# Kernel tuning notes

Hardware: AMD Instinct MI355X
Metric: run time of the kernel (lower is better)

The kernel has to match this reference:

```python
import jax, jax.numpy as jnp
import numpy as np

B, S, DM, H = 4, 4096, 1024, 16
HD = DM // H

def setup_inputs() -> dict:
    key = jax.random.key(0)
    ks = jax.random.split(key, 9)
    sc = 1.0 / np.sqrt(DM)
    return {
        "x": jax.random.normal(ks[0], (B, S, DM), dtype=jnp.float32),
        "Wq": jax.random.normal(ks[1], (DM, DM), dtype=jnp.float32) * sc,
        "bq": jnp.zeros((DM,), dtype=jnp.float32),
        "Wk": jax.random.normal(ks[2], (DM, DM), dtype=jnp.float32) * sc,
        "bk": jnp.zeros((DM,), dtype=jnp.float32),
        "Wv": jax.random.normal(ks[3], (DM, DM), dtype=jnp.float32) * sc,
        "bv": jnp.zeros((DM,), dtype=jnp.float32),
        "Wo": jax.random.normal(ks[4], (DM, DM), dtype=jnp.float32) * sc,
        "bo": jnp.zeros((DM,), dtype=jnp.float32),
    }

def _heads(t):
    # [B,S,DM] -> [B,H,S,HD]
    return t.reshape(B, S, H, HD).transpose(0, 2, 1, 3)

def reference(x, Wq, bq, Wk, bk, Wv, bv, Wo, bo):
    q = _heads(x @ Wq.T + bq)
    k = _heads(x @ Wk.T + bk)
    v = _heads(x @ Wv.T + bv)
    q = jax.nn.elu(q) + 1.0  # positive feature map
    k = jax.nn.elu(k) + 1.0
    # kv aggregation: [B,H,HD,HD]
    kv = jnp.einsum('bhsd,bhse->bhde', k, v)
    qkv = jnp.einsum('bhsd,bhde->bhse', q, kv)  # [B,H,S,HD]
    k_sum = k.sum(axis=2)  # [B,H,HD]
    normalizer = jnp.einsum('bhsd,bhd->bhs', q, k_sum) + 1e-6
    out = qkv / normalizer[..., None]
    out = out.transpose(0, 2, 1, 3).reshape(B, S, DM)
    return out @ Wo.T + bo  # dropout is identity in eval
```

## Files before the change

kernel.cpp:

```cpp
#include <hip/hip_runtime.h>
#include <math.h>

#define NROWS  16384
#define DMODEL 1024
#define NHEAD  16
#define HDIM   64
#define SEQ    4096
#define NBATCH 4
#define NBH    64
#define SCHUNK 16
#define M1     1048576u

typedef __attribute__((ext_vector_type(8))) short bf16x8;
typedef __attribute__((ext_vector_type(4))) float f32x4;

__device__ __forceinline__ unsigned short f2bf(float f) {
    unsigned u = __float_as_uint(f);
    u += 0x7FFFu + ((u >> 16) & 1u);
    return (unsigned short)(u >> 16);
}
__device__ __forceinline__ float bf2f(unsigned short h) {
    return __uint_as_float((unsigned)h << 16);
}

__device__ __forceinline__ void gload16(const void* g, void* l) {
    __builtin_amdgcn_global_load_lds(
        (const __attribute__((address_space(1))) unsigned int*)g,
        (__attribute__((address_space(3))) unsigned int*)l, 16, 0, 0);
}

__global__ __launch_bounds__(256)
void split_pair(const float* __restrict__ a, unsigned short* __restrict__ hi,
                unsigned short* __restrict__ lo, int n4)
{
    int i = blockIdx.x * 256 + threadIdx.x;
    const int stride = gridDim.x * 256;
    for (; i < n4; i += stride) {
        const float4 v = ((const float4*)a)[i];
        ushort4 H, L;
        H.x = f2bf(v.x); L.x = f2bf(v.x - bf2f(H.x));
        H.y = f2bf(v.y); L.y = f2bf(v.y - bf2f(H.y));
        H.z = f2bf(v.z); L.z = f2bf(v.z - bf2f(H.z));
        H.w = f2bf(v.w); L.w = f2bf(v.w - bf2f(H.w));
        ((ushort4*)hi)[i] = H;
        ((ushort4*)lo)[i] = L;
    }
}

__global__ __launch_bounds__(256)
void split_w4(const float* __restrict__ a0, const float* __restrict__ a1,
              const float* __restrict__ a2, const float* __restrict__ a3,
              unsigned short* __restrict__ dst)
{
    const int y = blockIdx.y;
    const float* src = (y == 0) ? a0 : (y == 1) ? a1 : (y == 2) ? a2 : a3;
    unsigned short* hi = dst + (size_t)y * 2u * M1;
    unsigned short* lo = hi + M1;
    const int i = blockIdx.x * 256 + threadIdx.x;
    const float4 v = ((const float4*)src)[i];
    ushort4 H, L;
    H.x = f2bf(v.x); L.x = f2bf(v.x - bf2f(H.x));
    H.y = f2bf(v.y); L.y = f2bf(v.y - bf2f(H.y));
    H.z = f2bf(v.z); L.z = f2bf(v.z - bf2f(H.z));
    H.w = f2bf(v.w); L.w = f2bf(v.w - bf2f(H.w));
    ((ushort4*)hi)[i] = H;
    ((ushort4*)lo)[i] = L;
}

template<int ELU>
__global__ __launch_bounds__(512)
void gemm_split8(const unsigned short* __restrict__ Ah, const unsigned short* __restrict__ Al,
                 const unsigned short* __restrict__ Wh, const unsigned short* __restrict__ Wl,
                 const float* __restrict__ bias, float* __restrict__ C)
{
    __shared__ unsigned short lds[2 * 32768];
    const int t    = threadIdx.x;
    const int lane = t & 63;
    const int wv   = t >> 6;
    const int wr   = wv >> 2;
    const int wcn  = wv & 3;

    const int bid  = blockIdx.x;
    const int swz  = ((bid & 7) << 5) | (bid >> 3);
    const int am0  = (swz >> 2) * 256;
    const int bn0  = (swz & 3) * 256;

    const int fr   = lane & 15;
    const int j0   = lane >> 4;
    const unsigned fro = (unsigned)((j0 * 16 + fr) * 8);
    const int srcr = lane & 15;
    const int srcc = (lane >> 4) * 8;

    f32x4 acc[8][4];
#pragma unroll
    for (int i = 0; i < 8; ++i)
#pragma unroll
        for (int j = 0; j < 4; ++j)
#pragma unroll
            for (int e = 0; e < 4; ++e) acc[i][j][e] = 0.f;

    auto stage = [&](int ph, int k0, unsigned wb) {
        const unsigned short* gs = (ph == 0) ? Ah : (ph == 1) ? Al : (ph == 2) ? Wh : Wl;
        const int rbase = (ph < 2) ? am0 : bn0;
#pragma unroll
        for (int c = 0; c < 2; ++c) {
            const int grow = rbase + c * 128 + wv * 16 + srcr;
            gload16(gs + (size_t)grow * DMODEL + k0 + srcc,
                    (unsigned short*)&lds[wb + (unsigned)ph * 8192u + (unsigned)(c * 8 + wv) * 512u]);
        }
    };

#pragma unroll
    for (int ph = 0; ph < 4; ++ph) stage(ph, 0, 0u);
    __syncthreads();

    for (int ks = 0; ks < 32; ++ks) {
        const unsigned rb = (ks & 1) ? 32768u : 0u;
        const unsigned wb = rb ^ 32768u;
        const int k0n = (ks + 1) * 32;
        const bool pf = (ks < 31);

        bf16x8 bh[4], bl[4];
#pragma unroll
        for (int ph = 0; ph < 4; ++ph) {
            if (ph == 0) {
#pragma unroll
                for (int j = 0; j < 4; ++j) {
                    const unsigned ch = (unsigned)(wcn * 4 + j) * 512u;
                    bh[j] = *(const bf16x8*)&lds[rb + 16384u + ch + fro];
                    bl[j] = *(const bf16x8*)&lds[rb + 24576u + ch + fro];
                }
            }
            bf16x8 a_h[2], a_l[2];
#pragma unroll
            for (int i2 = 0; i2 < 2; ++i2) {
                const unsigned ch = (unsigned)(wr * 8 + ph * 2 + i2) * 512u;
                a_h[i2] = *(const bf16x8*)&lds[rb + ch + fro];
                a_l[i2] = *(const bf16x8*)&lds[rb + 8192u + ch + fro];
            }
            if (pf) stage(ph, k0n, wb);
            __builtin_amdgcn_s_barrier();
            __builtin_amdgcn_s_setprio(1);
#pragma unroll
            for (int i2 = 0; i2 < 2; ++i2)
#pragma unroll
                for (int j = 0; j < 4; ++j) {
                    acc[ph * 2 + i2][j] = __builtin_amdgcn_mfma_f32_16x16x32_bf16(a_h[i2], bh[j], acc[ph * 2 + i2][j], 0, 0, 0);
                    acc[ph * 2 + i2][j] = __builtin_amdgcn_mfma_f32_16x16x32_bf16(a_h[i2], bl[j], acc[ph * 2 + i2][j], 0, 0, 0);
                    acc[ph * 2 + i2][j] = __builtin_amdgcn_mfma_f32_16x16x32_bf16(a_l[i2], bh[j], acc[ph * 2 + i2][j], 0, 0, 0);
                }
            __builtin_amdgcn_s_setprio(0);
            if (ph < 3) __builtin_amdgcn_s_barrier();
        }
        __syncthreads();
    }

    const int crow0 = am0 + wr * 128 + (lane >> 4) * 4;
    const int ccol0 = bn0 + wcn * 64 + fr;
#pragma unroll
    for (int j = 0; j < 4; ++j) {
        const int col = ccol0 + j * 16;
        const float bv = bias[col];
#pragma unroll
        for (int i = 0; i < 8; ++i) {
            const int row = crow0 + i * 16;
#pragma unroll
            for (int r = 0; r < 4; ++r) {
                float v = acc[i][j][r] + bv;
                if (ELU) v = (v > 0.f) ? (v + 1.f) : __expf(v);
                C[(size_t)(row + r) * DMODEL + col] = v;
            }
        }
    }
}

__global__ __launch_bounds__(512)
void kv_partial(const float* __restrict__ k, const float* __restrict__ v,
                float* __restrict__ kvp, float* __restrict__ ksp)
{
    __shared__ float Ks[32][64];
    __shared__ float Vs[32][64];
    const int t  = threadIdx.x;
    const int bh = blockIdx.x;
    const int b  = bh >> 4;
    const int h  = bh & 15;
    const int sc = blockIdx.y;
    const int d  = t & 63;
    const int e0 = (t >> 6) * 8;

    float acc[8];
#pragma unroll
    for (int j = 0; j < 8; ++j) acc[j] = 0.f;
    float ks = 0.f;

    const size_t rowbase = (size_t)b * SEQ;
    const int sbeg = sc * (SEQ / SCHUNK);
    const int send = sbeg + (SEQ / SCHUNK);
    const int lrow = t >> 4;
    const int lc4  = (t & 15) * 4;

    for (int s0 = sbeg; s0 < send; s0 += 32) {
        const size_t g = (rowbase + s0 + lrow) * DMODEL + h * HDIM + lc4;
        *(float4*)&Ks[lrow][lc4] = *(const float4*)&k[g];
        *(float4*)&Vs[lrow][lc4] = *(const float4*)&v[g];
        __syncthreads();
#pragma unroll 8
        for (int sp = 0; sp < 32; ++sp) {
            const float kd = Ks[sp][d];
            if (t < 64) ks += Ks[sp][t];
            const float4 v0 = *(const float4*)&Vs[sp][e0 + 0];
            const float4 v1 = *(const float4*)&Vs[sp][e0 + 4];
            acc[0] = fmaf(kd, v0.x, acc[0]);  acc[1] = fmaf(kd, v0.y, acc[1]);
            acc[2] = fmaf(kd, v0.z, acc[2]);  acc[3] = fmaf(kd, v0.w, acc[3]);
            acc[4] = fmaf(kd, v1.x, acc[4]);  acc[5] = fmaf(kd, v1.y, acc[5]);
            acc[6] = fmaf(kd, v1.z, acc[6]);  acc[7] = fmaf(kd, v1.w, acc[7]);
        }
        __syncthreads();
    }

    const size_t base = ((size_t)sc * NBH + bh) * HDIM;
    float4 o0; o0.x = acc[0]; o0.y = acc[1]; o0.z = acc[2]; o0.w = acc[3];
    float4 o1; o1.x = acc[4]; o1.y = acc[5]; o1.z = acc[6]; o1.w = acc[7];
    *(float4*)&kvp[(base + d) * HDIM + e0 + 0] = o0;
    *(float4*)&kvp[(base + d) * HDIM + e0 + 4] = o1;
    if (t < 64) ksp[base + t] = ks;
}

__global__ __launch_bounds__(256)
void kv_reduce(const float* __restrict__ kvp, const float* __restrict__ ksp,
               float* __restrict__ kv, float* __restrict__ ksum)
{
    const int i = blockIdx.x * 256 + threadIdx.x;
    const int NKV = NBH * HDIM * HDIM;
    if (i < NKV) {
        float s = 0.f;
#pragma unroll
        for (int c = 0; c < SCHUNK; ++c) s += kvp[(size_t)c * NKV + i];
        kv[i] = s;
    }
    if (i < NBH * HDIM) {
        float s = 0.f;
#pragma unroll
        for (int c = 0; c < SCHUNK; ++c) s += ksp[(size_t)c * NBH * HDIM + i];
        ksum[i] = s;
    }
}

__global__ __launch_bounds__(256)
void qkv_norm(const float* __restrict__ q, const float* __restrict__ kv,
              const float* __restrict__ ksum,
              unsigned short* __restrict__ ah, unsigned short* __restrict__ al)
{
    __shared__ float Qs[64][68];
    __shared__ float KVs[64][64];
    __shared__ float kss[64];
    const int t  = threadIdx.x;
    const int s0 = blockIdx.x * 64;
    const int b  = blockIdx.y;
    const int h  = blockIdx.z;
    const int bh = b * NHEAD + h;

#pragma unroll
    for (int i = 0; i < 4; ++i) {
        const int idx = i * 256 + t;
        const int row = idx >> 4;
        const int c4  = (idx & 15) * 4;
        const float4 vq = *(const float4*)&q[((size_t)b * SEQ + s0 + row) * DMODEL + h * HDIM + c4];
        *(float4*)&Qs[row][c4] = vq;
        *(float4*)&((float*)KVs)[idx * 4] = *(const float4*)&kv[(size_t)bh * HDIM * HDIM + idx * 4];
    }
    if (t < 64) kss[t] = ksum[(size_t)bh * HDIM + t];
    __syncthreads();

    const int r  = t >> 2;
    const int e0 = (t & 3) * 16;
    float out[16];
#pragma unroll
    for (int j = 0; j < 16; ++j) out[j] = 0.f;
    float nrm = 0.f;

#pragma unroll 8
    for (int d = 0; d < 64; ++d) {
        const float qd = Qs[r][d];
        nrm = fmaf(qd, kss[d], nrm);
        const float4 k0 = *(const float4*)&KVs[d][e0 + 0];
        const float4 k1 = *(const float4*)&KVs[d][e0 + 4];
        const float4 k2 = *(const float4*)&KVs[d][e0 + 8];
        const float4 k3 = *(const float4*)&KVs[d][e0 + 12];
        out[0]  = fmaf(qd, k0.x, out[0]);  out[1]  = fmaf(qd, k0.y, out[1]);
        out[2]  = fmaf(qd, k0.z, out[2]);  out[3]  = fmaf(qd, k0.w, out[3]);
        out[4]  = fmaf(qd, k1.x, out[4]);  out[5]  = fmaf(qd, k1.y, out[5]);
        out[6]  = fmaf(qd, k1.z, out[6]);  out[7]  = fmaf(qd, k1.w, out[7]);
        out[8]  = fmaf(qd, k2.x, out[8]);  out[9]  = fmaf(qd, k2.y, out[9]);
        out[10] = fmaf(qd, k2.z, out[10]); out[11] = fmaf(qd, k2.w, out[11]);
        out[12] = fmaf(qd, k3.x, out[12]); out[13] = fmaf(qd, k3.y, out[13]);
        out[14] = fmaf(qd, k3.z, out[14]); out[15] = fmaf(qd, k3.w, out[15]);
    }

    const float inv = 1.f / (nrm + 1e-6f);
    const size_t gbase = ((size_t)b * SEQ + s0 + r) * DMODEL + h * HDIM + e0;
#pragma unroll
    for (int g4 = 0; g4 < 4; ++g4) {
        ushort4 H, L;
        const float v0 = out[g4*4+0] * inv;
        const float v1 = out[g4*4+1] * inv;
        const float v2 = out[g4*4+2] * inv;
        const float v3 = out[g4*4+3] * inv;
        H.x = f2bf(v0); L.x = f2bf(v0 - bf2f(H.x));
        H.y = f2bf(v1); L.y = f2bf(v1 - bf2f(H.y));
        H.z = f2bf(v2); L.z = f2bf(v2 - bf2f(H.z));
        H.w = f2bf(v3); L.w = f2bf(v3 - bf2f(H.w));
        *(ushort4*)&ah[gbase + g4 * 4] = H;
        *(ushort4*)&al[gbase + g4 * 4] = L;
    }
}

extern "C" void kernel_launch(void* const* d_in, const int* in_sizes, int n_in,
                              void* d_out, int out_size, void* d_ws, size_t ws_size,
                              hipStream_t stream)
{
    const float* x  = (const float*)d_in[0];
    const float* Wq = (const float*)d_in[1];
    const float* bq = (const float*)d_in[2];
    const float* Wk = (const float*)d_in[3];
    const float* bk = (const float*)d_in[4];
    const float* Wv = (const float*)d_in[5];
    const float* bv = (const float*)d_in[6];
    const float* Wo = (const float*)d_in[7];
    const float* bo = (const float*)d_in[8];

    unsigned short* xh = (unsigned short*)d_ws;
    unsigned short* xl = xh + (size_t)NROWS * DMODEL;
    unsigned short* wsp = xl + (size_t)NROWS * DMODEL;
    float* buf0 = (float*)(wsp + 8u * M1);
    float* kv   = buf0 + (size_t)NROWS * DMODEL;
    float* ksum = kv + NBH * HDIM * HDIM;
    float* kvp  = ksum + NBH * HDIM;
    float* ksp  = kvp + (size_t)SCHUNK * NBH * HDIM * HDIM;
    float* vbuf = (float*)d_out;

    const dim3 gg(256);
    const int n4x = NROWS * DMODEL / 4;

    split_w4<<<dim3(1024, 4), 256, 0, stream>>>(Wq, Wk, Wv, Wo, wsp);
    split_pair<<<4096, 256, 0, stream>>>(x, xh, xl, n4x);
    gemm_split8<1><<<gg, 512, 0, stream>>>(xh, xl, wsp + 2u * M1, wsp + 3u * M1, bk, buf0);
    gemm_split8<0><<<gg, 512, 0, stream>>>(xh, xl, wsp + 4u * M1, wsp + 5u * M1, bv, vbuf);
    kv_partial<<<dim3(NBH, SCHUNK), 512, 0, stream>>>(buf0, vbuf, kvp, ksp);
    kv_reduce<<<1024, 256, 0, stream>>>(kvp, ksp, kv, ksum);
    gemm_split8<1><<<gg, 512, 0, stream>>>(xh, xl, wsp, wsp + M1, bq, buf0);
    qkv_norm<<<dim3(SEQ / 64, NBATCH, NHEAD), 256, 0, stream>>>(buf0, kv, ksum, xh, xl);
    gemm_split8<0><<<gg, 512, 0, stream>>>(xh, xl, wsp + 6u * M1, wsp + 7u * M1, bo, (float*)d_out);
}
```

Before: 488.2 us.

## Rewrite split-bf16 GEMM with triple-buffered LDS, smaller tiles, fused K/V launch

The GEMM moves to 256x128 tiles and a three-stage LDS ring. Loads are issued two k-steps ahead and gated by explicit vmcnt waits, replacing the per-phase barriers of the old double-buffered loop. Weights are packed into contiguous hi and lo arrays, so the K and V projections run as one launch over a concatenated 2048-column weight, with ELU and the output destination chosen per column block. Smaller tiles give twice as many blocks for better occupancy and load balance, at the cost of more operand re-reads and a larger LDS footprint per block.

```diff
diff --git a/kernel.cpp b/kernel.cpp
--- a/kernel.cpp
+++ b/kernel.cpp
@@ -13,6 +13,10 @@
 
 typedef __attribute__((ext_vector_type(8))) short bf16x8;
 typedef __attribute__((ext_vector_type(4))) float f32x4;
+
+#define VMCNT(N) asm volatile("s_waitcnt vmcnt(" #N ")" ::: "memory")
+#define BAR() do { asm volatile("" ::: "memory"); __builtin_amdgcn_s_barrier(); \
+                   asm volatile("" ::: "memory"); } while (0)
 
 __device__ __forceinline__ unsigned short f2bf(float f) {
     unsigned u = __float_as_uint(f);
@@ -50,12 +54,10 @@
 __global__ __launch_bounds__(256)
 void split_w4(const float* __restrict__ a0, const float* __restrict__ a1,
               const float* __restrict__ a2, const float* __restrict__ a3,
-              unsigned short* __restrict__ dst)
+              unsigned short* __restrict__ hib, unsigned short* __restrict__ lob)
 {
     const int y = blockIdx.y;
     const float* src = (y == 0) ? a0 : (y == 1) ? a1 : (y == 2) ? a2 : a3;
-    unsigned short* hi = dst + (size_t)y * 2u * M1;
-    unsigned short* lo = hi + M1;
     const int i = blockIdx.x * 256 + threadIdx.x;
     const float4 v = ((const float4*)src)[i];
     ushort4 H, L;
@@ -63,27 +65,32 @@
     H.y = f2bf(v.y); L.y = f2bf(v.y - bf2f(H.y));
     H.z = f2bf(v.z); L.z = f2bf(v.z - bf2f(H.z));
     H.w = f2bf(v.w); L.w = f2bf(v.w - bf2f(H.w));
-    ((ushort4*)hi)[i] = H;
-    ((ushort4*)lo)[i] = L;
-}
-
-template<int ELU>
+    const size_t o = (size_t)y * M1 + (size_t)i * 4;
+    *(ushort4*)&hib[o] = H;
+    *(ushort4*)&lob[o] = L;
+}
+
+template<int MODE>
 __global__ __launch_bounds__(512)
-void gemm_split8(const unsigned short* __restrict__ Ah, const unsigned short* __restrict__ Al,
-                 const unsigned short* __restrict__ Wh, const unsigned short* __restrict__ Wl,
-                 const float* __restrict__ bias, float* __restrict__ C)
-{
-    __shared__ unsigned short lds[2 * 32768];
+void gemm_t3(const unsigned short* __restrict__ Ah, const unsigned short* __restrict__ Al,
+             const unsigned short* __restrict__ WhB, const unsigned short* __restrict__ WlB,
+             const float* __restrict__ bias0, const float* __restrict__ bias1,
+             float* __restrict__ C0, float* __restrict__ C1, int nbs, int wrow0)
+{
+    __shared__ unsigned short lds[73728];
     const int t    = threadIdx.x;
     const int lane = t & 63;
     const int wv   = t >> 6;
-    const int wr   = wv >> 2;
-    const int wcn  = wv & 3;
+    const int wr   = wv >> 1;
+    const int wcn  = wv & 1;
 
     const int bid  = blockIdx.x;
-    const int swz  = ((bid & 7) << 5) | (bid >> 3);
-    const int am0  = (swz >> 2) * 256;
-    const int bn0  = (swz & 3) * 256;
+    const int swz  = (bid & 7) * ((int)gridDim.x >> 3) + (bid >> 3);
+    const int NBm  = (1 << nbs) - 1;
+    const int mb   = swz >> nbs;
+    const int nb   = swz & NBm;
+    const int am0  = mb * 256;
+    const int bn0g = wrow0 + nb * 128;
 
     const int fr   = lane & 15;
     const int j0   = lane >> 4;
@@ -91,84 +98,93 @@
     const int srcr = lane & 15;
     const int srcc = (lane >> 4) * 8;
 
-    f32x4 acc[8][4];
-#pragma unroll
-    for (int i = 0; i < 8; ++i)
+    f32x4 acc[4][4];
+#pragma unroll
+    for (int i = 0; i < 4; ++i)
 #pragma unroll
         for (int j = 0; j < 4; ++j)
 #pragma unroll
             for (int e = 0; e < 4; ++e) acc[i][j][e] = 0.f;
 
-    auto stage = [&](int ph, int k0, unsigned wb) {
-        const unsigned short* gs = (ph == 0) ? Ah : (ph == 1) ? Al : (ph == 2) ? Wh : Wl;
-        const int rbase = (ph < 2) ? am0 : bn0;
+    auto stage_full = [&](int kt, unsigned wb) {
 #pragma unroll
         for (int c = 0; c < 2; ++c) {
-            const int grow = rbase + c * 128 + wv * 16 + srcr;
-            gload16(gs + (size_t)grow * DMODEL + k0 + srcc,
-                    (unsigned short*)&lds[wb + (unsigned)ph * 8192u + (unsigned)(c * 8 + wv) * 512u]);
-        }
+            const int ch = wv * 2 + c;
+            const size_t ga = (size_t)(am0 + ch * 16 + srcr) * DMODEL + kt * 32 + srcc;
+            gload16(Ah + ga, (unsigned short*)&lds[wb + (unsigned)ch * 512u]);
+            gload16(Al + ga, (unsigned short*)&lds[wb + 8192u + (unsigned)ch * 512u]);
+        }
+        const size_t gb = (size_t)(bn0g + wv * 16 + srcr) * DMODEL + kt * 32 + srcc;
+        gload16(WhB + gb, (unsigned short*)&lds[wb + 16384u + (unsigned)wv * 512u]);
+        gload16(WlB + gb, (unsigned short*)&lds[wb + 20480u + (unsigned)wv * 512u]);
     };
 
-#pragma unroll
-    for (int ph = 0; ph < 4; ++ph) stage(ph, 0, 0u);
-    __syncthreads();
-
-    for (int ks = 0; ks < 32; ++ks) {
-        const unsigned rb = (ks & 1) ? 32768u : 0u;
-        const unsigned wb = rb ^ 32768u;
-        const int k0n = (ks + 1) * 32;
-        const bool pf = (ks < 31);
-
+    auto phases = [&](unsigned rd, unsigned wb, int k2, bool doStage) {
         bf16x8 bh[4], bl[4];
 #pragma unroll
-        for (int ph = 0; ph < 4; ++ph) {
-            if (ph == 0) {
-#pragma unroll
-                for (int j = 0; j < 4; ++j) {
-                    const unsigned ch = (unsigned)(wcn * 4 + j) * 512u;
-                    bh[j] = *(const bf16x8*)&lds[rb + 16384u + ch + fro];
-                    bl[j] = *(const bf16x8*)&lds[rb + 24576u + ch + fro];
+        for (int j = 0; j < 4; ++j) {
+            const unsigned ch = (unsigned)(wcn * 4 + j) * 512u;
+            bh[j] = *(const bf16x8*)&lds[rd + 16384u + ch + fro];
+            bl[j] = *(const bf16x8*)&lds[rd + 20480u + ch + fro];
+        }
+#pragma unroll
+        for (int p = 0; p < 4; ++p) {
+            const unsigned ch = (unsigned)(wr * 4 + p) * 512u;
+            const bf16x8 a_h = *(const bf16x8*)&lds[rd + ch + fro];
+            const bf16x8 a_l = *(const bf16x8*)&lds[rd + 8192u + ch + fro];
+            if (doStage) {
+                if (p < 2) {
+                    const int cch = wv * 2 + p;
+                    const size_t ga = (size_t)(am0 + cch * 16 + srcr) * DMODEL + k2 * 32 + srcc;
+                    gload16(Ah + ga, (unsigned short*)&lds[wb + (unsigned)cch * 512u]);
+                    gload16(Al + ga, (unsigned short*)&lds[wb + 8192u + (unsigned)cch * 512u]);
+                } else if (p == 2) {
+                    const size_t gb = (size_t)(bn0g + wv * 16 + srcr) * DMODEL + k2 * 32 + srcc;
+                    gload16(WhB + gb, (unsigned short*)&lds[wb + 16384u + (unsigned)wv * 512u]);
+                    gload16(WlB + gb, (unsigned short*)&lds[wb + 20480u + (unsigned)wv * 512u]);
                 }
             }
-            bf16x8 a_h[2], a_l[2];
-#pragma unroll
-            for (int i2 = 0; i2 < 2; ++i2) {
-                const unsigned ch = (unsigned)(wr * 8 + ph * 2 + i2) * 512u;
-                a_h[i2] = *(const bf16x8*)&lds[rb + ch + fro];
-                a_l[i2] = *(const bf16x8*)&lds[rb + 8192u + ch + fro];
+            __builtin_amdgcn_s_setprio(1);
+#pragma unroll
+            for (int j = 0; j < 4; ++j) {
+                acc[p][j] = __builtin_amdgcn_mfma_f32_16x16x32_bf16(a_h, bh[j], acc[p][j], 0, 0, 0);
+                acc[p][j] = __builtin_amdgcn_mfma_f32_16x16x32_bf16(a_h, bl[j], acc[p][j], 0, 0, 0);
+                acc[p][j] = __builtin_amdgcn_mfma_f32_16x16x32_bf16(a_l, bh[j], acc[p][j], 0, 0, 0);
             }
-            if (pf) stage(ph, k0n, wb);
-            __builtin_amdgcn_s_barrier();
-            __builtin_amdgcn_s_setprio(1);
-#pragma unroll
-            for (int i2 = 0; i2 < 2; ++i2)
-#pragma unroll
-                for (int j = 0; j < 4; ++j) {
-                    acc[ph * 2 + i2][j] = __builtin_amdgcn_mfma_f32_16x16x32_bf16(a_h[i2], bh[j], acc[ph * 2 + i2][j], 0, 0, 0);
-                    acc[ph * 2 + i2][j] = __builtin_amdgcn_mfma_f32_16x16x32_bf16(a_h[i2], bl[j], acc[ph * 2 + i2][j], 0, 0, 0);
-                    acc[ph * 2 + i2][j] = __builtin_amdgcn_mfma_f32_16x16x32_bf16(a_l[i2], bh[j], acc[ph * 2 + i2][j], 0, 0, 0);
-                }
             __builtin_amdgcn_s_setprio(0);
-            if (ph < 3) __builtin_amdgcn_s_barrier();
-        }
-        __syncthreads();
-    }
-
-    const int crow0 = am0 + wr * 128 + (lane >> 4) * 4;
-    const int ccol0 = bn0 + wcn * 64 + fr;
+        }
+    };
+
+    stage_full(0, 0u);
+    stage_full(1, 24576u);
+
+    for (int kt = 0; kt < 30; kt += 3) {
+        VMCNT(6); BAR(); phases(0u,     49152u, kt + 2, true);
+        VMCNT(6); BAR(); phases(24576u, 0u,     kt + 3, true);
+        VMCNT(6); BAR(); phases(49152u, 24576u, kt + 4, true);
+    }
+    VMCNT(6); BAR(); phases(0u,     0u, 0, false);
+    VMCNT(0); BAR(); phases(24576u, 0u, 0, false);
+
+    const bool elu = (MODE == 1) || (MODE == 2 && nb < 8);
+    float* Cm = C0;
+    const float* bm = bias0;
+    int coff = 0;
+    if (MODE == 2 && nb >= 8) { Cm = C1; bm = bias1; coff = 1024; }
+    const int crow0 = am0 + wr * 64 + (lane >> 4) * 4;
+    const int ccol0 = nb * 128 + wcn * 64 + fr - coff;
 #pragma unroll
     for (int j = 0; j < 4; ++j) {
         const int col = ccol0 + j * 16;
-        const float bv = bias[col];
-#pragma unroll
-        for (int i = 0; i < 8; ++i) {
+        const float bv = bm[col];
+#pragma unroll
+        for (int i = 0; i < 4; ++i) {
             const int row = crow0 + i * 16;
 #pragma unroll
             for (int r = 0; r < 4; ++r) {
                 float v = acc[i][j][r] + bv;
-                if (ELU) v = (v > 0.f) ? (v + 1.f) : __expf(v);
-                C[(size_t)(row + r) * DMODEL + col] = v;
+                if (elu) v = (v > 0.f) ? (v + 1.f) : __expf(v);
+                Cm[(size_t)(row + r) * DMODEL + col] = v;
             }
         }
     }
@@ -329,26 +345,25 @@
     const float* Wo = (const float*)d_in[7];
     const float* bo = (const float*)d_in[8];
 
-    unsigned short* xh = (unsigned short*)d_ws;
-    unsigned short* xl = xh + (size_t)NROWS * DMODEL;
-    unsigned short* wsp = xl + (size_t)NROWS * DMODEL;
-    float* buf0 = (float*)(wsp + 8u * M1);
+    unsigned short* xh  = (unsigned short*)d_ws;
+    unsigned short* xl  = xh + (size_t)NROWS * DMODEL;
+    unsigned short* hib = xl + (size_t)NROWS * DMODEL;
+    unsigned short* lob = hib + 4u * M1;
+    float* buf0 = (float*)(lob + 4u * M1);
     float* kv   = buf0 + (size_t)NROWS * DMODEL;
     float* ksum = kv + NBH * HDIM * HDIM;
     float* kvp  = ksum + NBH * HDIM;
     float* ksp  = kvp + (size_t)SCHUNK * NBH * HDIM * HDIM;
     float* vbuf = (float*)d_out;
 
-    const dim3 gg(256);
     const int n4x = NROWS * DMODEL / 4;
 
-    split_w4<<<dim3(1024, 4), 256, 0, stream>>>(Wq, Wk, Wv, Wo, wsp);
+    split_w4<<<dim3(1024, 4), 256, 0, stream>>>(Wq, Wk, Wv, Wo, hib, lob);
     split_pair<<<4096, 256, 0, stream>>>(x, xh, xl, n4x);
-    gemm_split8<1><<<gg, 512, 0, stream>>>(xh, xl, wsp + 2u * M1, wsp + 3u * M1, bk, buf0);
-    gemm_split8<0><<<gg, 512, 0, stream>>>(xh, xl, wsp + 4u * M1, wsp + 5u * M1, bv, vbuf);
+    gemm_t3<2><<<1024, 512, 0, stream>>>(xh, xl, hib, lob, bk, bv, buf0, vbuf, 4, 1024);
     kv_partial<<<dim3(NBH, SCHUNK), 512, 0, stream>>>(buf0, vbuf, kvp, ksp);
     kv_reduce<<<1024, 256, 0, stream>>>(kvp, ksp, kv, ksum);
-    gemm_split8<1><<<gg, 512, 0, stream>>>(xh, xl, wsp, wsp + M1, bq, buf0);
+    gemm_t3<1><<<512, 512, 0, stream>>>(xh, xl, hib, lob, bq, nullptr, buf0, nullptr, 3, 0);
     qkv_norm<<<dim3(SEQ / 64, NBATCH, NHEAD), 256, 0, stream>>>(buf0, kv, ksum, xh, xl);
-    gemm_split8<0><<<gg, 512, 0, stream>>>(xh, xl, wsp + 6u * M1, wsp + 7u * M1, bo, (float*)d_out);
-}
+    gemm_t3<0><<<512, 512, 0, stream>>>(xh, xl, hib, lob, bo, nullptr, (float*)d_out, nullptr, 3, 3072);
+}
```

Result: slower. 551.2 us (+12.9%).

## Deepen GEMM load pipeline with partial vmcnt waits and early W prefetch

Applied to the files above, without the earlier changes.

Reworks the split-bf16 GEMM's global-to-LDS staging so the weight tiles are prefetched two k-steps ahead and the activation tiles one step ahead. W tiles are written into the buffer currently being read, which is safe because their fragments are already in registers after phase 0. The full __syncthreads at the end of each k-step, which drains all outstanding loads, is replaced by an explicit s_waitcnt vmcnt(4) plus a barrier at the top of the step. This lets later loads stay in flight while the current tile is consumed, hiding more memory latency. The cost is tighter reliance on hand-counted vmcnt ordering and buffer-reuse correctness.

```diff
diff --git a/kernel.cpp b/kernel.cpp
--- a/kernel.cpp
+++ b/kernel.cpp
@@ -13,6 +13,10 @@
 
 typedef __attribute__((ext_vector_type(8))) short bf16x8;
 typedef __attribute__((ext_vector_type(4))) float f32x4;
+
+#define VMCNT(N) asm volatile("s_waitcnt vmcnt(" #N ")" ::: "memory")
+#define BAR() do { asm volatile("" ::: "memory"); __builtin_amdgcn_s_barrier(); \
+                   asm volatile("" ::: "memory"); } while (0)
 
 __device__ __forceinline__ unsigned short f2bf(float f) {
     unsigned u = __float_as_uint(f);
@@ -69,9 +73,9 @@
 
 template<int ELU>
 __global__ __launch_bounds__(512)
-void gemm_split8(const unsigned short* __restrict__ Ah, const unsigned short* __restrict__ Al,
-                 const unsigned short* __restrict__ Wh, const unsigned short* __restrict__ Wl,
-                 const float* __restrict__ bias, float* __restrict__ C)
+void gemm_cp(const unsigned short* __restrict__ Ah, const unsigned short* __restrict__ Al,
+             const unsigned short* __restrict__ Wh, const unsigned short* __restrict__ Wl,
+             const float* __restrict__ bias, float* __restrict__ C)
 {
     __shared__ unsigned short lds[2 * 32768];
     const int t    = threadIdx.x;
@@ -99,26 +103,27 @@
 #pragma unroll
             for (int e = 0; e < 4; ++e) acc[i][j][e] = 0.f;
 
-    auto stage = [&](int ph, int k0, unsigned wb) {
-        const unsigned short* gs = (ph == 0) ? Ah : (ph == 1) ? Al : (ph == 2) ? Wh : Wl;
-        const int rbase = (ph < 2) ? am0 : bn0;
+    auto stage_op = [&](int kt, int op) {
+        if (kt >= 32) return;
+        const unsigned short* gs = (op == 0) ? Ah : (op == 1) ? Al : (op == 2) ? Wh : Wl;
+        const int rbase = (op < 2) ? am0 : bn0;
+        const int k0 = kt * 32;
+        const unsigned wb = ((unsigned)kt & 1u) * 32768u + (unsigned)op * 8192u;
 #pragma unroll
         for (int c = 0; c < 2; ++c) {
             const int grow = rbase + c * 128 + wv * 16 + srcr;
             gload16(gs + (size_t)grow * DMODEL + k0 + srcc,
-                    (unsigned short*)&lds[wb + (unsigned)ph * 8192u + (unsigned)(c * 8 + wv) * 512u]);
+                    (unsigned short*)&lds[wb + (unsigned)(c * 8 + wv) * 512u]);
         }
     };
 
-#pragma unroll
-    for (int ph = 0; ph < 4; ++ph) stage(ph, 0, 0u);
-    __syncthreads();
+    stage_op(0, 2); stage_op(0, 3); stage_op(0, 0); stage_op(0, 1);
+    stage_op(1, 2); stage_op(1, 3);
 
     for (int ks = 0; ks < 32; ++ks) {
-        const unsigned rb = (ks & 1) ? 32768u : 0u;
-        const unsigned wb = rb ^ 32768u;
-        const int k0n = (ks + 1) * 32;
-        const bool pf = (ks < 31);
+        const unsigned rb = ((unsigned)ks & 1u) * 32768u;
+        if (ks < 31) { VMCNT(4); } else { VMCNT(0); }
+        BAR();
 
         bf16x8 bh[4], bl[4];
 #pragma unroll
@@ -138,7 +143,10 @@
                 a_h[i2] = *(const bf16x8*)&lds[rb + ch + fro];
                 a_l[i2] = *(const bf16x8*)&lds[rb + 8192u + ch + fro];
             }
-            if (pf) stage(ph, k0n, wb);
+            if (ph == 0)      stage_op(ks + 1, 0);
+            else if (ph == 1) stage_op(ks + 1, 1);
+            else if (ph == 2) stage_op(ks + 2, 2);
+            else              stage_op(ks + 2, 3);
             __builtin_amdgcn_s_barrier();
             __builtin_amdgcn_s_setprio(1);
 #pragma unroll
@@ -152,7 +160,6 @@
             __builtin_amdgcn_s_setprio(0);
             if (ph < 3) __builtin_amdgcn_s_barrier();
         }
-        __syncthreads();
     }
 
     const int crow0 = am0 + wr * 128 + (lane >> 4) * 4;
@@ -344,11 +351,11 @@
 
     split_w4<<<dim3(1024, 4), 256, 0, stream>>>(Wq, Wk, Wv, Wo, wsp);
     split_pair<<<4096, 256, 0, stream>>>(x, xh, xl, n4x);
-    gemm_split8<1><<<gg, 512, 0, stream>>>(xh, xl, wsp + 2u * M1, wsp + 3u * M1, bk, buf0);
-    gemm_split8<0><<<gg, 512, 0, stream>>>(xh, xl, wsp + 4u * M1, wsp + 5u * M1, bv, vbuf);
+    gemm_cp<1><<<gg, 512, 0, stream>>>(xh, xl, wsp + 2u * M1, wsp + 3u * M1, bk, buf0);
+    gemm_cp<0><<<gg, 512, 0, stream>>>(xh, xl, wsp + 4u * M1, wsp + 5u * M1, bv, vbuf);
     kv_partial<<<dim3(NBH, SCHUNK), 512, 0, stream>>>(buf0, vbuf, kvp, ksp);
     kv_reduce<<<1024, 256, 0, stream>>>(kvp, ksp, kv, ksum);
-    gemm_split8<1><<<gg, 512, 0, stream>>>(xh, xl, wsp, wsp + M1, bq, buf0);
+    gemm_cp<1><<<gg, 512, 0, stream>>>(xh, xl, wsp, wsp + M1, bq, buf0);
     qkv_norm<<<dim3(SEQ / 64, NBATCH, NHEAD), 256, 0, stream>>>(buf0, kv, ksum, xh, xl);
-    gemm_split8<0><<<gg, 512, 0, stream>>>(xh, xl, wsp + 6u * M1, wsp + 7u * M1, bo, (float*)d_out);
-}
+    gemm_cp<0><<<gg, 512, 0, stream>>>(xh, xl, wsp + 6u * M1, wsp + 7u * M1, bo, (float*)d_out);
+}
```

New measurement: 493.5 us. No clear change (+1.1%).
